# Performance work log

Hardware: AMD Instinct MI355X
Metric: run time of the kernel (lower is better)

The kernel has to match this reference:

```python
import jax, jax.numpy as jnp
import numpy as np

NEG_BIG = -1e10
EPS = 1e-12  # F.normalize default eps


def l2_normalize(x, axis=-1):
    # matches torch.nn.functional.normalize(x): x / max(||x||_2, eps)
    n = jnp.sqrt(jnp.sum(x * x, axis=axis, keepdims=True))
    return x / jnp.maximum(n, EPS)


def setup_inputs() -> dict:
    key = jax.random.key(0)
    k1, k2, k3 = jax.random.split(key, 3)
    B, S, T, D, R = 16, 512, 512, 512, 8
    return {
        "src_emb": jax.random.normal(k1, (B, S, D), dtype=jnp.float32),
        "tar_emb": jax.random.normal(k2, (B, T, D), dtype=jnp.float32),
        "src_mask": jnp.ones((B, S), dtype=jnp.float32),
        "tar_mask": jnp.ones((B, T), dtype=jnp.float32),
        "mul_score_w": jax.random.normal(k3, (R, D), dtype=jnp.float32),
    }


def reference(src_emb, tar_emb, src_mask, tar_mask, mul_score_w):
    # w: [R, D] row-normalized relation vectors
    w = l2_normalize(mul_score_w, axis=-1)
    # rank-1 diagonal projections per relation
    src_wt = jnp.einsum("bsd,rd->brs", src_emb, w)          # [B,R,S]
    tar_wt = jnp.einsum("btd,rd->brt", tar_emb, w)          # [B,R,T]
    src_map = src_wt[..., None] * w[None, :, None, :]        # [B,R,S,D]
    tar_map = tar_wt[..., None] * w[None, :, None, :]        # [B,R,T,D]
    # attention scores per relation
    score = jnp.einsum("brsd,brtd->brst", src_map, tar_map)  # [B,R,S,T]
    pair_mask = src_mask[:, :, None] * tar_mask[:, None, :]  # [B,S,T]
    score = score + ((1.0 - pair_mask) * NEG_BIG)[:, None, :, :]
    weight = jax.nn.softmax(score, axis=3)                   # softmax over tar
    # sum over rel and tar in one contraction (avoids 5D tensor)
    out = jnp.einsum("brst,brtd->bsd", weight, tar_map)      # [B,S,D]
    return out
```

## Files before the change

kernel.cpp:

```cpp
#include <hip/hip_runtime.h>
#include <hip/hip_bf16.h>
#include <math.h>

#define B 16
#define Sn 512
#define Tn 512
#define Dn 512
#define Rn 8
#define NEG_BIG (-1e10f)
#define L2E 1.4426950408889634f

__device__ __forceinline__ float dot4(float4 a, float4 b) {
  return a.x * b.x + a.y * b.y + a.z * b.z + a.w * b.w;
}

__device__ __forceinline__ float fold_reduce8(const float* p, int lane) {
  bool b0 = lane & 1;
  float q[4];
#pragma unroll
  for (int j = 0; j < 4; ++j) {
    float s = b0 ? p[2 * j] : p[2 * j + 1];
    float rv = __shfl_xor(s, 1, 64);
    q[j] = (b0 ? p[2 * j + 1] : p[2 * j]) + rv;
  }
  bool b1 = lane & 2;
  float u[2];
#pragma unroll
  for (int j = 0; j < 2; ++j) {
    float s = b1 ? q[2 * j] : q[2 * j + 1];
    float rv = __shfl_xor(s, 2, 64);
    u[j] = (b1 ? q[2 * j + 1] : q[2 * j]) + rv;
  }
  bool b2 = lane & 4;
  float s = b2 ? u[0] : u[1];
  float rv = __shfl_xor(s, 4, 64);
  float v = (b2 ? u[1] : u[0]) + rv;
  v += __shfl_xor(v, 8, 64);
  v += __shfl_xor(v, 16, 64);
  v += __shfl_xor(v, 32, 64);
  return v;
}

__device__ __forceinline__ void load_norm_w(const float* __restrict__ w,
                                            int lane, float4* wa, float4* wb,
                                            float* g) {
  const float4* wg = (const float4*)w;
  float ss[8];
#pragma unroll
  for (int r = 0; r < 8; ++r) {
    wa[r] = wg[r * 128 + lane];
    wb[r] = wg[r * 128 + 64 + lane];
    ss[r] = dot4(wa[r], wa[r]) + dot4(wb[r], wb[r]);
  }
#pragma unroll
  for (int off = 32; off; off >>= 1) {
#pragma unroll
    for (int r = 0; r < 8; ++r) ss[r] += __shfl_xor(ss[r], off, 64);
  }
#pragma unroll
  for (int r = 0; r < 8; ++r) {
    float iv = 1.0f / fmaxf(sqrtf(ss[r]), 1e-12f);
    wa[r].x *= iv; wa[r].y *= iv; wa[r].z *= iv; wa[r].w *= iv;
    wb[r].x *= iv; wb[r].y *= iv; wb[r].z *= iv; wb[r].w *= iv;
    g[r] = ss[r] * iv * iv;
  }
}

__global__ __launch_bounds__(256) void proj_kernel(
    const float* __restrict__ src_emb, const float* __restrict__ tar_emb,
    const float* __restrict__ w, float* __restrict__ src_wt,
    float* __restrict__ tar_wt) {
  int lane = threadIdx.x & 63, wid = threadIdx.x >> 6;
  float4 wa[8], wb[8];
  float g[8];
  load_norm_w(w, lane, wa, wb, g);

  int row0 = blockIdx.x * 16 + wid * 4;
  bool is_src = row0 < B * Sn;
  const float* emb = is_src ? src_emb : tar_emb;
  float* wt = is_src ? src_wt : tar_wt;
  int rb = is_src ? row0 : row0 - B * Sn;

  float v[4];
#pragma unroll
  for (int i = 0; i < 4; ++i) {
    const float4* e4 = (const float4*)(emb + (size_t)(rb + i) * Dn);
    float4 xa = e4[lane];
    float4 xb = e4[64 + lane];
    float p[8];
#pragma unroll
    for (int r = 0; r < 8; ++r) p[r] = dot4(xa, wa[r]) + dot4(xb, wb[r]);
    v[i] = fold_reduce8(p, lane);
  }
  if (lane < 32) {
    int ri = lane >> 3;
    float val = (ri == 0) ? v[0] : (ri == 1) ? v[1] : (ri == 2) ? v[2] : v[3];
    wt[(size_t)(rb + ri) * 8 + (lane & 7)] = val;
  }
}

__global__ __launch_bounds__(256) void fused_kernel(
    const float* __restrict__ src_wt, const float* __restrict__ tar_wt,
    const float* __restrict__ src_mask, const float* __restrict__ tar_mask,
    const float* __restrict__ w, float* __restrict__ out) {
  __shared__ __align__(16) float tw_lds[Tn * 12];
  __shared__ float tm_lds[Tn];
  __shared__ __align__(16) float cacc_lds[16 * 8];
  __shared__ float mred[4];

  int lane = threadIdx.x & 63, wid = threadIdx.x >> 6;
  int b = blockIdx.x >> 5;
  int s0 = (blockIdx.x & 31) * 16;

  float4 wa[8], wb[8];
  float g[8];
  load_norm_w(w, lane, wa, wb, g);

  const float4* twg = (const float4*)(tar_wt + (size_t)b * Tn * 8);
  float mloc = 0.0f;
#pragma unroll
  for (int k = 0; k < 4; ++k) {
    int idx = k * 256 + threadIdx.x;
    float4 vv = twg[idx];
    int t = idx >> 1, hf = idx & 1;
    *(float4*)&tw_lds[t * 12 + hf * 4] = vv;
    mloc = fmaxf(mloc, fmaxf(fmaxf(fabsf(vv.x), fabsf(vv.y)),
                             fmaxf(fabsf(vv.z), fabsf(vv.w))));
  }
  for (int k = threadIdx.x; k < Tn; k += 256)
    tm_lds[k] = tar_mask[b * Tn + k];
#pragma unroll
  for (int off = 32; off; off >>= 1)
    mloc = fmaxf(mloc, __shfl_xor(mloc, off, 64));
  if (lane == 0) mred[wid] = mloc;
  __syncthreads();
  float M = fmaxf(fmaxf(mred[0], mred[1]), fmaxf(mred[2], mred[3]));

  int r = lane & 7, h = (lane >> 3) & 1, sl4 = lane >> 4;
  int s_local = wid * 4 + sl4;
  int s = s0 + s_local;

  float g_r = (r & 4) ? ((r & 2) ? ((r & 1) ? g[7] : g[6])
                                 : ((r & 1) ? g[5] : g[4]))
                      : ((r & 2) ? ((r & 1) ? g[3] : g[2])
                                 : ((r & 1) ? g[1] : g[0]));
  float sw = src_wt[((size_t)(b * Sn + s)) * 8 + r];
  float sm = src_mask[b * Sn + s];
  float a = g_r * sw;
  float A2 = a * L2E;
  float Bm = sm * (-NEG_BIG) * L2E;
  float C2 = L2E * (sm * NEG_BIG - fabsf(a) * M);

  float ps = 0.0f, wsum = 0.0f;
  int t0 = h * 256;
#pragma unroll 8
  for (int t = t0; t < t0 + 256; ++t) {
    float tw = tw_lds[t * 12 + r];
    float tm = tm_lds[t];
    float sc = fmaf(A2, tw, fmaf(Bm, tm, C2));
    float p = __builtin_amdgcn_exp2f(sc);
    ps += p;
    wsum = fmaf(p, tw, wsum);
  }
  ps += __shfl_xor(ps, 8, 64);
  wsum += __shfl_xor(wsum, 8, 64);
  if (h == 0) cacc_lds[s_local * 8 + r] = wsum / ps;
  __syncthreads();

#pragma unroll
  for (int i = 0; i < 4; ++i) {
    int srow = wid * 4 + i;
    float4 c0 = *(const float4*)&cacc_lds[srow * 8];
    float4 c1 = *(const float4*)&cacc_lds[srow * 8 + 4];
    float cc[8] = {c0.x, c0.y, c0.z, c0.w, c1.x, c1.y, c1.z, c1.w};
    float4 o0 = {0, 0, 0, 0}, o1 = {0, 0, 0, 0};
#pragma unroll
    for (int rr = 0; rr < 8; ++rr) {
      o0.x = fmaf(cc[rr], wa[rr].x, o0.x);
      o0.y = fmaf(cc[rr], wa[rr].y, o0.y);
      o0.z = fmaf(cc[rr], wa[rr].z, o0.z);
      o0.w = fmaf(cc[rr], wa[rr].w, o0.w);
      o1.x = fmaf(cc[rr], wb[rr].x, o1.x);
      o1.y = fmaf(cc[rr], wb[rr].y, o1.y);
      o1.z = fmaf(cc[rr], wb[rr].z, o1.z);
      o1.w = fmaf(cc[rr], wb[rr].w, o1.w);
    }
    float4* dst = (float4*)(out + (size_t)(b * Sn + s0 + srow) * Dn);
    dst[lane] = o0;
    dst[64 + lane] = o1;
  }
}

extern "C" void kernel_launch(void* const* d_in, const int* in_sizes, int n_in,
                              void* d_out, int out_size, void* d_ws,
                              size_t ws_size, hipStream_t stream) {
  const float* src_emb = (const float*)d_in[0];
  const float* tar_emb = (const float*)d_in[1];
  const float* src_mask = (const float*)d_in[2];
  const float* tar_mask = (const float*)d_in[3];
  const float* w_in = (const float*)d_in[4];
  float* out = (float*)d_out;

  float* ws = (float*)d_ws;
  float* src_wt = ws;
  float* tar_wt = ws + 65536;

  proj_kernel<<<(B * (Sn + Tn)) / 16, 256, 0, stream>>>(src_emb, tar_emb, w_in,
                                                        src_wt, tar_wt);
  fused_kernel<<<B * (Sn / 16), 256, 0, stream>>>(src_wt, tar_wt, src_mask,
                                                  tar_mask, w_in, out);
}
```

Before: 102.3 us.

## Merge projection and attention kernels into one cooperative launch with grid sync

Fuses the projection and fused attention kernels into a single cooperative kernel of 512 blocks that separates the phases with a grid-wide barrier, so the second launch and its normalized-weight reload go away. Each phase-1 block now handles 32 rows, with two rows interleaved per iteration. If the cooperative launch fails, the code falls back to two regular launches. The grid barrier costs synchronization time, and the large LDS footprint limits blocks per CU, which could reduce phase-1 occupancy.

```diff
diff --git a/kernel.cpp b/kernel.cpp
--- a/kernel.cpp
+++ b/kernel.cpp
@@ -1,6 +1,9 @@
 #include <hip/hip_runtime.h>
+#include <hip/hip_cooperative_groups.h>
 #include <hip/hip_bf16.h>
 #include <math.h>
+
+namespace cg = cooperative_groups;
 
 #define B 16
 #define Sn 512
@@ -9,6 +12,8 @@
 #define Rn 8
 #define NEG_BIG (-1e10f)
 #define L2E 1.4426950408889634f
+
+#define NBLK 512
 
 __device__ __forceinline__ float dot4(float4 a, float4 b) {
   return a.x * b.x + a.y * b.y + a.z * b.z + a.w * b.w;
@@ -66,69 +71,64 @@
   }
 }
 
-__global__ __launch_bounds__(256) void proj_kernel(
-    const float* __restrict__ src_emb, const float* __restrict__ tar_emb,
-    const float* __restrict__ w, float* __restrict__ src_wt,
-    float* __restrict__ tar_wt) {
-  int lane = threadIdx.x & 63, wid = threadIdx.x >> 6;
-  float4 wa[8], wb[8];
-  float g[8];
-  load_norm_w(w, lane, wa, wb, g);
-
-  int row0 = blockIdx.x * 16 + wid * 4;
+__device__ __forceinline__ void phase1(int blk, int tid,
+                                       const float* __restrict__ src_emb,
+                                       const float* __restrict__ tar_emb,
+                                       const float4* wa, const float4* wb,
+                                       float* __restrict__ src_wt,
+                                       float* __restrict__ tar_wt) {
+  int lane = tid & 63, wid = tid >> 6;
+  int row0 = blk * 32 + wid * 8;
   bool is_src = row0 < B * Sn;
   const float* emb = is_src ? src_emb : tar_emb;
   float* wt = is_src ? src_wt : tar_wt;
   int rb = is_src ? row0 : row0 - B * Sn;
 
-  float v[4];
-#pragma unroll
-  for (int i = 0; i < 4; ++i) {
-    const float4* e4 = (const float4*)(emb + (size_t)(rb + i) * Dn);
-    float4 xa = e4[lane];
-    float4 xb = e4[64 + lane];
-    float p[8];
-#pragma unroll
-    for (int r = 0; r < 8; ++r) p[r] = dot4(xa, wa[r]) + dot4(xb, wb[r]);
-    v[i] = fold_reduce8(p, lane);
-  }
-  if (lane < 32) {
-    int ri = lane >> 3;
-    float val = (ri == 0) ? v[0] : (ri == 1) ? v[1] : (ri == 2) ? v[2] : v[3];
-    wt[(size_t)(rb + ri) * 8 + (lane & 7)] = val;
-  }
-}
-
-__global__ __launch_bounds__(256) void fused_kernel(
-    const float* __restrict__ src_wt, const float* __restrict__ tar_wt,
-    const float* __restrict__ src_mask, const float* __restrict__ tar_mask,
-    const float* __restrict__ w, float* __restrict__ out) {
-  __shared__ __align__(16) float tw_lds[Tn * 12];
-  __shared__ float tm_lds[Tn];
-  __shared__ __align__(16) float cacc_lds[16 * 8];
-  __shared__ float mred[4];
-
-  int lane = threadIdx.x & 63, wid = threadIdx.x >> 6;
-  int b = blockIdx.x >> 5;
-  int s0 = (blockIdx.x & 31) * 16;
-
-  float4 wa[8], wb[8];
-  float g[8];
-  load_norm_w(w, lane, wa, wb, g);
+#pragma unroll
+  for (int i = 0; i < 8; i += 2) {
+    const float4* e0 = (const float4*)(emb + (size_t)(rb + i) * Dn);
+    const float4* e1 = (const float4*)(emb + (size_t)(rb + i + 1) * Dn);
+    float4 x0a = e0[lane], x0b = e0[64 + lane];
+    float4 x1a = e1[lane], x1b = e1[64 + lane];
+    float p0[8], p1[8];
+#pragma unroll
+    for (int r = 0; r < 8; ++r) {
+      p0[r] = dot4(x0a, wa[r]) + dot4(x0b, wb[r]);
+      p1[r] = dot4(x1a, wa[r]) + dot4(x1b, wb[r]);
+    }
+    float v0 = fold_reduce8(p0, lane);
+    float v1 = fold_reduce8(p1, lane);
+    if (lane < 8) wt[(size_t)(rb + i) * 8 + lane] = v0;
+    else if (lane < 16) wt[(size_t)(rb + i + 1) * 8 + (lane & 7)] = v1;
+  }
+}
+
+__device__ __forceinline__ void phase2(int blk, int tid,
+                                       const float* __restrict__ src_wt,
+                                       const float* __restrict__ tar_wt,
+                                       const float* __restrict__ src_mask,
+                                       const float* __restrict__ tar_mask,
+                                       const float4* wa, const float4* wb,
+                                       const float* g,
+                                       float* __restrict__ out, float* tw_lds,
+                                       float* tm_lds, float* cacc_lds,
+                                       float* mred) {
+  int lane = tid & 63, wid = tid >> 6;
+  int b = blk >> 5;
+  int s0 = (blk & 31) * 16;
 
   const float4* twg = (const float4*)(tar_wt + (size_t)b * Tn * 8);
   float mloc = 0.0f;
 #pragma unroll
   for (int k = 0; k < 4; ++k) {
-    int idx = k * 256 + threadIdx.x;
+    int idx = k * 256 + tid;
     float4 vv = twg[idx];
     int t = idx >> 1, hf = idx & 1;
     *(float4*)&tw_lds[t * 12 + hf * 4] = vv;
     mloc = fmaxf(mloc, fmaxf(fmaxf(fabsf(vv.x), fabsf(vv.y)),
                              fmaxf(fabsf(vv.z), fabsf(vv.w))));
   }
-  for (int k = threadIdx.x; k < Tn; k += 256)
-    tm_lds[k] = tar_mask[b * Tn + k];
+  for (int k = tid; k < Tn; k += 256) tm_lds[k] = tar_mask[b * Tn + k];
 #pragma unroll
   for (int off = 32; off; off >>= 1)
     mloc = fmaxf(mloc, __shfl_xor(mloc, off, 64));
@@ -191,6 +191,54 @@
   }
 }
 
+__global__ __launch_bounds__(256) void mulrel_coop(
+    const float* __restrict__ src_emb, const float* __restrict__ tar_emb,
+    const float* __restrict__ src_mask, const float* __restrict__ tar_mask,
+    const float* __restrict__ w, float* __restrict__ src_wt,
+    float* __restrict__ tar_wt, float* __restrict__ out) {
+  __shared__ __align__(16) float tw_lds[Tn * 12];
+  __shared__ float tm_lds[Tn];
+  __shared__ __align__(16) float cacc_lds[16 * 8];
+  __shared__ float mred[4];
+
+  int lane = threadIdx.x & 63;
+  float4 wa[8], wb[8];
+  float g[8];
+  load_norm_w(w, lane, wa, wb, g);
+
+  phase1(blockIdx.x, threadIdx.x, src_emb, tar_emb, wa, wb, src_wt, tar_wt);
+  cg::this_grid().sync();
+  phase2(blockIdx.x, threadIdx.x, src_wt, tar_wt, src_mask, tar_mask, wa, wb,
+         g, out, tw_lds, tm_lds, cacc_lds, mred);
+}
+
+__global__ __launch_bounds__(256) void k_phase1(
+    const float* __restrict__ src_emb, const float* __restrict__ tar_emb,
+    const float* __restrict__ w, float* __restrict__ src_wt,
+    float* __restrict__ tar_wt) {
+  int lane = threadIdx.x & 63;
+  float4 wa[8], wb[8];
+  float g[8];
+  load_norm_w(w, lane, wa, wb, g);
+  phase1(blockIdx.x, threadIdx.x, src_emb, tar_emb, wa, wb, src_wt, tar_wt);
+}
+
+__global__ __launch_bounds__(256) void k_phase2(
+    const float* __restrict__ src_wt, const float* __restrict__ tar_wt,
+    const float* __restrict__ src_mask, const float* __restrict__ tar_mask,
+    const float* __restrict__ w, float* __restrict__ out) {
+  __shared__ __align__(16) float tw_lds[Tn * 12];
+  __shared__ float tm_lds[Tn];
+  __shared__ __align__(16) float cacc_lds[16 * 8];
+  __shared__ float mred[4];
+  int lane = threadIdx.x & 63;
+  float4 wa[8], wb[8];
+  float g[8];
+  load_norm_w(w, lane, wa, wb, g);
+  phase2(blockIdx.x, threadIdx.x, src_wt, tar_wt, src_mask, tar_mask, wa, wb,
+         g, out, tw_lds, tm_lds, cacc_lds, mred);
+}
+
 extern "C" void kernel_launch(void* const* d_in, const int* in_sizes, int n_in,
                               void* d_out, int out_size, void* d_ws,
                               size_t ws_size, hipStream_t stream) {
@@ -205,8 +253,14 @@
   float* src_wt = ws;
   float* tar_wt = ws + 65536;
 
-  proj_kernel<<<(B * (Sn + Tn)) / 16, 256, 0, stream>>>(src_emb, tar_emb, w_in,
-                                                        src_wt, tar_wt);
-  fused_kernel<<<B * (Sn / 16), 256, 0, stream>>>(src_wt, tar_wt, src_mask,
-                                                  tar_mask, w_in, out);
-}
+  void* args[] = {(void*)&src_emb, (void*)&tar_emb, (void*)&src_mask,
+                  (void*)&tar_mask, (void*)&w_in,   (void*)&src_wt,
+                  (void*)&tar_wt,   (void*)&out};
+  hipError_t err = hipLaunchCooperativeKernel(
+      (void*)mulrel_coop, dim3(NBLK), dim3(256), args, 0, stream);
+  if (err != hipSuccess) {
+    k_phase1<<<NBLK, 256, 0, stream>>>(src_emb, tar_emb, w_in, src_wt, tar_wt);
+    k_phase2<<<NBLK, 256, 0, stream>>>(src_wt, tar_wt, src_mask, tar_mask,
+                                       w_in, out);
+  }
+}
```

New measurement: 157.4 us. 1.54x slower.

## Halve rows per block and split target loop across warps with transposed LDS

Applied to the files above, without the earlier changes.

The projection kernel now handles 2 rows per wave instead of 4, doubling its grid. The fused kernel processes 8 source rows per block, so the grid doubles. Each of its four waves covers a quarter of the target range, reading from a transposed, padded LDS layout with float4 loads, and the partial sums are reduced through shared memory. The aim is more parallelism and fewer LDS instructions in the exp loop. In exchange it adds an extra barrier and cross-wave reduction, and w is loaded and normalized again in twice as many blocks.

```diff
diff --git a/kernel.cpp b/kernel.cpp
--- a/kernel.cpp
+++ b/kernel.cpp
@@ -6,9 +6,9 @@
 #define Sn 512
 #define Tn 512
 #define Dn 512
-#define Rn 8
 #define NEG_BIG (-1e10f)
 #define L2E 1.4426950408889634f
+#define TW_STRIDE 516
 
 __device__ __forceinline__ float dot4(float4 a, float4 b) {
   return a.x * b.x + a.y * b.y + a.z * b.z + a.w * b.w;
@@ -66,7 +66,7 @@
   }
 }
 
-__global__ __launch_bounds__(256) void proj_kernel(
+__global__ __launch_bounds__(256) void k_phase1(
     const float* __restrict__ src_emb, const float* __restrict__ tar_emb,
     const float* __restrict__ w, float* __restrict__ src_wt,
     float* __restrict__ tar_wt) {
@@ -75,42 +75,41 @@
   float g[8];
   load_norm_w(w, lane, wa, wb, g);
 
-  int row0 = blockIdx.x * 16 + wid * 4;
+  int row0 = blockIdx.x * 8 + wid * 2;
   bool is_src = row0 < B * Sn;
   const float* emb = is_src ? src_emb : tar_emb;
   float* wt = is_src ? src_wt : tar_wt;
   int rb = is_src ? row0 : row0 - B * Sn;
 
-  float v[4];
-#pragma unroll
-  for (int i = 0; i < 4; ++i) {
-    const float4* e4 = (const float4*)(emb + (size_t)(rb + i) * Dn);
-    float4 xa = e4[lane];
-    float4 xb = e4[64 + lane];
-    float p[8];
-#pragma unroll
-    for (int r = 0; r < 8; ++r) p[r] = dot4(xa, wa[r]) + dot4(xb, wb[r]);
-    v[i] = fold_reduce8(p, lane);
-  }
-  if (lane < 32) {
-    int ri = lane >> 3;
-    float val = (ri == 0) ? v[0] : (ri == 1) ? v[1] : (ri == 2) ? v[2] : v[3];
-    wt[(size_t)(rb + ri) * 8 + (lane & 7)] = val;
-  }
-}
-
-__global__ __launch_bounds__(256) void fused_kernel(
+  const float4* e0 = (const float4*)(emb + (size_t)rb * Dn);
+  const float4* e1 = (const float4*)(emb + (size_t)(rb + 1) * Dn);
+  float4 x0a = e0[lane], x0b = e0[64 + lane];
+  float4 x1a = e1[lane], x1b = e1[64 + lane];
+  float p0[8], p1[8];
+#pragma unroll
+  for (int r = 0; r < 8; ++r) {
+    p0[r] = dot4(x0a, wa[r]) + dot4(x0b, wb[r]);
+    p1[r] = dot4(x1a, wa[r]) + dot4(x1b, wb[r]);
+  }
+  float v0 = fold_reduce8(p0, lane);
+  float v1 = fold_reduce8(p1, lane);
+  if (lane < 8) wt[(size_t)rb * 8 + lane] = v0;
+  else if (lane < 16) wt[(size_t)(rb + 1) * 8 + (lane & 7)] = v1;
+}
+
+__global__ __launch_bounds__(256, 4) void k_phase2(
     const float* __restrict__ src_wt, const float* __restrict__ tar_wt,
     const float* __restrict__ src_mask, const float* __restrict__ tar_mask,
     const float* __restrict__ w, float* __restrict__ out) {
-  __shared__ __align__(16) float tw_lds[Tn * 12];
-  __shared__ float tm_lds[Tn];
-  __shared__ __align__(16) float cacc_lds[16 * 8];
+  __shared__ float tw_lds[8 * TW_STRIDE];
+  __shared__ __align__(16) float tm_lds[Tn];
+  __shared__ float red_ps[4][64], red_ws[4][64];
+  __shared__ float cacc[64];
   __shared__ float mred[4];
 
-  int lane = threadIdx.x & 63, wid = threadIdx.x >> 6;
-  int b = blockIdx.x >> 5;
-  int s0 = (blockIdx.x & 31) * 16;
+  int tid = threadIdx.x, lane = tid & 63, wid = tid >> 6;
+  int b = blockIdx.x >> 6;
+  int s0 = (blockIdx.x & 63) * 8;
 
   float4 wa[8], wb[8];
   float g[8];
@@ -120,15 +119,18 @@
   float mloc = 0.0f;
 #pragma unroll
   for (int k = 0; k < 4; ++k) {
-    int idx = k * 256 + threadIdx.x;
+    int idx = k * 256 + tid;
     float4 vv = twg[idx];
-    int t = idx >> 1, hf = idx & 1;
-    *(float4*)&tw_lds[t * 12 + hf * 4] = vv;
+    int t = idx >> 1, h = idx & 1;
+    tw_lds[(4 * h + 0) * TW_STRIDE + t] = vv.x;
+    tw_lds[(4 * h + 1) * TW_STRIDE + t] = vv.y;
+    tw_lds[(4 * h + 2) * TW_STRIDE + t] = vv.z;
+    tw_lds[(4 * h + 3) * TW_STRIDE + t] = vv.w;
     mloc = fmaxf(mloc, fmaxf(fmaxf(fabsf(vv.x), fabsf(vv.y)),
                              fmaxf(fabsf(vv.z), fabsf(vv.w))));
   }
-  for (int k = threadIdx.x; k < Tn; k += 256)
-    tm_lds[k] = tar_mask[b * Tn + k];
+  if (tid < 128)
+    *(float4*)&tm_lds[tid * 4] = ((const float4*)(tar_mask + b * Tn))[tid];
 #pragma unroll
   for (int off = 32; off; off >>= 1)
     mloc = fmaxf(mloc, __shfl_xor(mloc, off, 64));
@@ -136,15 +138,14 @@
   __syncthreads();
   float M = fmaxf(fmaxf(mred[0], mred[1]), fmaxf(mred[2], mred[3]));
 
-  int r = lane & 7, h = (lane >> 3) & 1, sl4 = lane >> 4;
-  int s_local = wid * 4 + sl4;
-  int s = s0 + s_local;
+  int r = lane & 7, sl = lane >> 3;
+  int s = s0 + sl;
 
   float g_r = (r & 4) ? ((r & 2) ? ((r & 1) ? g[7] : g[6])
                                  : ((r & 1) ? g[5] : g[4]))
                       : ((r & 2) ? ((r & 1) ? g[3] : g[2])
                                  : ((r & 1) ? g[1] : g[0]));
-  float sw = src_wt[((size_t)(b * Sn + s)) * 8 + r];
+  float sw = src_wt[((size_t)(b * Sn + s0)) * 8 + lane];
   float sm = src_mask[b * Sn + s];
   float a = g_r * sw;
   float A2 = a * L2E;
@@ -152,27 +153,40 @@
   float C2 = L2E * (sm * NEG_BIG - fabsf(a) * M);
 
   float ps = 0.0f, wsum = 0.0f;
-  int t0 = h * 256;
+  const float* twr = &tw_lds[r * TW_STRIDE + wid * 128];
+  const float* tmr = &tm_lds[wid * 128];
 #pragma unroll 8
-  for (int t = t0; t < t0 + 256; ++t) {
-    float tw = tw_lds[t * 12 + r];
-    float tm = tm_lds[t];
-    float sc = fmaf(A2, tw, fmaf(Bm, tm, C2));
-    float p = __builtin_amdgcn_exp2f(sc);
-    ps += p;
-    wsum = fmaf(p, tw, wsum);
-  }
-  ps += __shfl_xor(ps, 8, 64);
-  wsum += __shfl_xor(wsum, 8, 64);
-  if (h == 0) cacc_lds[s_local * 8 + r] = wsum / ps;
+  for (int i = 0; i < 32; ++i) {
+    float4 tw4 = *(const float4*)&twr[i * 4];
+    float4 tm4 = *(const float4*)&tmr[i * 4];
+    float sc, p;
+    sc = fmaf(A2, tw4.x, fmaf(Bm, tm4.x, C2));
+    p = __builtin_amdgcn_exp2f(sc); ps += p; wsum = fmaf(p, tw4.x, wsum);
+    sc = fmaf(A2, tw4.y, fmaf(Bm, tm4.y, C2));
+    p = __builtin_amdgcn_exp2f(sc); ps += p; wsum = fmaf(p, tw4.y, wsum);
+    sc = fmaf(A2, tw4.z, fmaf(Bm, tm4.z, C2));
+    p = __builtin_amdgcn_exp2f(sc); ps += p; wsum = fmaf(p, tw4.z, wsum);
+    sc = fmaf(A2, tw4.w, fmaf(Bm, tm4.w, C2));
+    p = __builtin_amdgcn_exp2f(sc); ps += p; wsum = fmaf(p, tw4.w, wsum);
+  }
+  red_ps[wid][lane] = ps;
+  red_ws[wid][lane] = wsum;
   __syncthreads();
-
-#pragma unroll
-  for (int i = 0; i < 4; ++i) {
-    int srow = wid * 4 + i;
-    float4 c0 = *(const float4*)&cacc_lds[srow * 8];
-    float4 c1 = *(const float4*)&cacc_lds[srow * 8 + 4];
-    float cc[8] = {c0.x, c0.y, c0.z, c0.w, c1.x, c1.y, c1.z, c1.w};
+  if (wid == 0) {
+    float pst = red_ps[0][lane] + red_ps[1][lane] + red_ps[2][lane] +
+                red_ps[3][lane];
+    float wst = red_ws[0][lane] + red_ws[1][lane] + red_ws[2][lane] +
+                red_ws[3][lane];
+    cacc[lane] = wst / pst;
+  }
+  __syncthreads();
+
+#pragma unroll
+  for (int i = 0; i < 2; ++i) {
+    int srow = wid * 2 + i;
+    float cc[8];
+#pragma unroll
+    for (int rr = 0; rr < 8; ++rr) cc[rr] = cacc[srow * 8 + rr];
     float4 o0 = {0, 0, 0, 0}, o1 = {0, 0, 0, 0};
 #pragma unroll
     for (int rr = 0; rr < 8; ++rr) {
@@ -205,8 +219,8 @@
   float* src_wt = ws;
   float* tar_wt = ws + 65536;
 
-  proj_kernel<<<(B * (Sn + Tn)) / 16, 256, 0, stream>>>(src_emb, tar_emb, w_in,
-                                                        src_wt, tar_wt);
-  fused_kernel<<<B * (Sn / 16), 256, 0, stream>>>(src_wt, tar_wt, src_mask,
-                                                  tar_mask, w_in, out);
-}
+  k_phase1<<<(B * (Sn + Tn)) / 8, 256, 0, stream>>>(src_emb, tar_emb, w_in,
+                                                    src_wt, tar_wt);
+  k_phase2<<<B * (Sn / 8), 256, 0, stream>>>(src_wt, tar_wt, src_mask,
+                                             tar_mask, w_in, out);
+}
```

After: 103.1 us. Within noise of the previous version (+0.7%).
